# Performance work log

Measured on AMD Instinct MI355X. Metric: run time of the kernel, lower is better.

The kernel has to match this reference:

```python
import jax, jax.numpy as jnp
import numpy as np

NUM_EMBEDDINGS = 16384
EMBED_DIM = 2048
B, C, H, W = 8, EMBED_DIM, 32, 32


def setup_inputs() -> dict:
    key = jax.random.key(0)
    k1, k2 = jax.random.split(key)
    hidden_state = jax.random.normal(k1, (B, C, H, W), dtype=jnp.float32)
    embedding = jax.random.normal(k2, (NUM_EMBEDDINGS, EMBED_DIM), dtype=jnp.float32)
    return {"hidden_state": hidden_state, "embedding": embedding}


def _l2_normalize(x, axis=-1, eps=1e-12):
    # matches torch F.normalize(p=2): x / max(||x||, eps)
    n = jnp.sqrt(jnp.sum(x * x, axis=axis, keepdims=True))
    return x / jnp.maximum(n, eps)


def reference(hidden_state, embedding):
    b, c, h, w = hidden_state.shape
    # (B,C,H,W) -> (B*H*W, C)
    flat = jnp.transpose(hidden_state, (0, 2, 3, 1)).reshape(-1, c)
    z = _l2_normalize(flat)                      # [N, D]
    e = _l2_normalize(embedding)                 # [K, D]
    sim = jnp.matmul(z, e.T)                     # [N, K]
    idx = jnp.argmax(sim, axis=1)                # [N]
    quant = e[idx]                               # [N, D]
    quant = quant.reshape(b, h, w, c).transpose(0, 3, 1, 2)
    return quant, idx
```

## Files before the change

### kernel.cpp

```cpp
#include <hip/hip_runtime.h>
#include <hip/hip_bf16.h>

#define NQ   8192
#define NK   16384
#define DIM  2048
#define KTILES 128
#define QUANT_ELEMS (8*2048*32*32)

typedef __attribute__((ext_vector_type(8))) short bf16x8;
typedef __attribute__((ext_vector_type(4))) float f32x4;

__device__ __forceinline__ void async16(const void* g, void* lds) {
  __builtin_amdgcn_global_load_lds(
      (const __attribute__((address_space(1))) unsigned int*)g,
      (__attribute__((address_space(3))) unsigned int*)lds,
      16, 0, 0);
}

__device__ __forceinline__ void t2_add(float v, int i,
                                       float& v1, int& i1, float& v2, int& i2) {
  if (v > v1) { v2 = v1; i2 = i1; v1 = v; i1 = i; }
  else if (v > v2) { v2 = v; i2 = i; }
}

__global__ __launch_bounds__(256) void norm_e_kernel(
    const float* __restrict__ e, __hip_bfloat16* __restrict__ eh,
    float* __restrict__ enorm) {
  const int k = blockIdx.x;
  const int t = threadIdx.x;
  const float* row = e + (size_t)k * DIM;
  float v[8];
  double ss = 0.0;
#pragma unroll
  for (int j = 0; j < 8; j++) { v[j] = row[t + 256 * j]; ss += (double)v[j] * (double)v[j]; }
  for (int s = 32; s; s >>= 1) ss += __shfl_down(ss, s);
  __shared__ double sb[4];
  __shared__ float snorm;
  if ((t & 63) == 0) sb[t >> 6] = ss;
  __syncthreads();
  if (t == 0) {
    snorm = fmaxf((float)sqrt(sb[0] + sb[1] + sb[2] + sb[3]), 1e-12f);
    enorm[k] = snorm;
  }
  __syncthreads();
  const float nf = snorm;
#pragma unroll
  for (int j = 0; j < 8; j++)
    eh[(size_t)k * DIM + t + 256 * j] = __float2bfloat16(v[j] / nf);
}

__global__ __launch_bounds__(256) void norm_z_kernel(
    const float* __restrict__ hid, __hip_bfloat16* __restrict__ zh) {
  const int bh = blockIdx.x;
  const int b = bh >> 5, h = bh & 31;
  const int n0 = bh * 32;
  const int t = threadIdx.x;
  const int w = t & 31, cp = t >> 5;

  __shared__ double ssq[8][32];
  __shared__ float nrm[32];
  __shared__ float tile[32][65];

  double acc = 0.0;
  const float* base = hid + ((size_t)b * DIM) * 1024 + h * 32 + w;
#pragma unroll 8
  for (int k = 0; k < 256; k++) {
    float val = base[(size_t)(cp * 256 + k) * 1024];
    acc += (double)val * (double)val;
  }
  ssq[cp][w] = acc;
  __syncthreads();
  if (t < 32) {
    double s = 0.0;
#pragma unroll
    for (int j = 0; j < 8; j++) s += ssq[j][t];
    nrm[t] = fmaxf((float)sqrt(s), 1e-12f);
  }
  __syncthreads();

  for (int ct = 0; ct < 32; ct++) {
    const int c0 = ct * 64;
#pragma unroll
    for (int jt = 0; jt < 8; jt++) {
      const int cl = jt * 8 + cp;
      tile[w][cl] = base[(size_t)(c0 + cl) * 1024];
    }
    __syncthreads();
#pragma unroll
    for (int it = 0; it < 8; it++) {
      const int nl = it * 4 + (t >> 6);
      const int cl = t & 63;
      zh[(size_t)(n0 + nl) * DIM + c0 + cl] =
          __float2bfloat16(tile[nl][cl] / nrm[nl]);
    }
    __syncthreads();
  }
}

__global__ __launch_bounds__(256) void gemm_top2(
    const __hip_bfloat16* __restrict__ A, const __hip_bfloat16* __restrict__ B,
    float4* __restrict__ pertile ) {
  __shared__ __align__(16) __hip_bfloat16 As[128 * 64];
  __shared__ __align__(16) __hip_bfloat16 Bs[128 * 64];

  const int nb = blockIdx.x;
  const int kb = blockIdx.y;
  const int n0 = nb * 128;
  const int k0 = kb * 128;

  const int tid  = threadIdx.x;
  const int wid  = tid >> 6;
  const int lane = tid & 63;
  const int wm = wid >> 1, wn = wid & 1;

  const int lr = lane >> 3;
  const int sc = ((lane & 7) ^ lr) * 8;

  f32x4 acc[4][4];
#pragma unroll
  for (int i = 0; i < 4; i++)
#pragma unroll
    for (int j = 0; j < 4; j++) acc[i][j] = (f32x4){0.f, 0.f, 0.f, 0.f};

  for (int d0 = 0; d0 < DIM; d0 += 64) {
    __syncthreads();
#pragma unroll
    for (int p = 0; p < 4; p++) {
      const int row = p * 32 + wid * 8 + lr;
      const __hip_bfloat16* ga = A + (size_t)(n0 + row) * DIM + d0 + sc;
      const __hip_bfloat16* gb = B + (size_t)(k0 + row) * DIM + d0 + sc;
      async16(ga, (char*)As + p * 4096 + wid * 1024);
      async16(gb, (char*)Bs + p * 4096 + wid * 1024);
    }
    __syncthreads();
#pragma unroll
    for (int kk = 0; kk < 2; kk++) {
      bf16x8 af[4], bfr[4];
      const int cg = kk * 4 + (lane >> 4);
#pragma unroll
      for (int mi = 0; mi < 4; mi++) {
        int r = wm * 64 + mi * 16 + (lane & 15);
        af[mi] = *(const bf16x8*)(As + r * 64 + ((cg ^ (r & 7)) * 8));
      }
#pragma unroll
      for (int ni = 0; ni < 4; ni++) {
        int r = wn * 64 + ni * 16 + (lane & 15);
        bfr[ni] = *(const bf16x8*)(Bs + r * 64 + ((cg ^ (r & 7)) * 8));
      }
#pragma unroll
      for (int mi = 0; mi < 4; mi++)
#pragma unroll
        for (int ni = 0; ni < 4; ni++)
          acc[mi][ni] = __builtin_amdgcn_mfma_f32_16x16x32_bf16(
              af[mi], bfr[ni], acc[mi][ni], 0, 0, 0);
    }
  }

  __syncthreads();
  float4* buf = (float4*)As;
  const int cbase = k0 + wn * 64 + (lane & 15);
#pragma unroll
  for (int mi = 0; mi < 4; mi++) {
#pragma unroll
    for (int j = 0; j < 4; j++) {
      float v1 = -INFINITY, v2 = -INFINITY;
      int i1 = -1, i2 = -1;
#pragma unroll
      for (int ni = 0; ni < 4; ni++)
        t2_add(acc[mi][ni][j], cbase + ni * 16, v1, i1, v2, i2);
      for (int s = 1; s < 16; s <<= 1) {
        float ov1 = __shfl_xor(v1, s); int oi1 = __shfl_xor(i1, s);
        float ov2 = __shfl_xor(v2, s); int oi2 = __shfl_xor(i2, s);
        t2_add(ov1, oi1, v1, i1, v2, i2);
        t2_add(ov2, oi2, v1, i1, v2, i2);
      }
      if ((lane & 15) == 0) {
        int rl = wm * 64 + mi * 16 + ((lane >> 4) << 2) + j;
        buf[rl * 2 + wn] = make_float4(v1, v2, __int_as_float(i1), __int_as_float(i2));
      }
    }
  }
  __syncthreads();
  if (tid < 128) {
    float4 a = buf[tid * 2 + 0], b = buf[tid * 2 + 1];
    float v1 = a.x, v2 = a.y;
    int i1 = __float_as_int(a.z), i2 = __float_as_int(a.w);
    t2_add(b.x, __float_as_int(b.z), v1, i1, v2, i2);
    t2_add(b.y, __float_as_int(b.w), v1, i1, v2, i2);
    pertile[(size_t)(n0 + tid) * KTILES + kb] =
        make_float4(v1, v2, __int_as_float(i1), __int_as_float(i2));
  }
}

#define DELTA 2e-3f
__global__ __launch_bounds__(256) void rescore_kernel(
    const float4* __restrict__ pertile, const float* __restrict__ hid,
    const float* __restrict__ emb, float* __restrict__ idx_f,
    int* __restrict__ idx_i) {
  const int n = blockIdx.x;
  const int t = threadIdx.x;
  __shared__ double sredd[2][4];
  __shared__ float sm[4];
  __shared__ int sl[128];
  __shared__ int scnt;

  float4 e4 = (t < 128) ? pertile[(size_t)n * KTILES + t]
                        : make_float4(-INFINITY, -INFINITY, 0.f, 0.f);
  float m = e4.x;
  for (int s = 32; s; s >>= 1) m = fmaxf(m, __shfl_xor(m, s));
  if ((t & 63) == 0) sm[t >> 6] = m;
  __syncthreads();
  if (t == 0) {
    sm[0] = fmaxf(fmaxf(sm[0], sm[1]), fmaxf(sm[2], sm[3]));
    scnt = 0;
  }
  __syncthreads();
  const float thr = sm[0] - DELTA;
  if (t < 128) {
    if (e4.x >= thr) { int p = atomicAdd(&scnt, 1); if (p < 128) sl[p] = __float_as_int(e4.z); }
    if (e4.y >= thr) { int p = atomicAdd(&scnt, 1); if (p < 128) sl[p] = __float_as_int(e4.w); }
  }
  __syncthreads();
  const int cnt = min(scnt, 128);

  const int b = n >> 10, hw = n & 1023;
  const float* zbase = hid + (size_t)b * DIM * 1024 + hw;
  double zv[8];
#pragma unroll
  for (int j = 0; j < 8; j++) zv[j] = (double)zbase[(size_t)(t + 256 * j) * 1024];

  double bestv = -1e300;
  int besti = 0x7fffffff;
  for (int c = 0; c < cnt; c++) {
    const int k = sl[c];
    const float* erow = emb + (size_t)k * DIM;
    double dot = 0.0, ee = 0.0;
#pragma unroll
    for (int j = 0; j < 8; j++) {
      double ev = (double)erow[t + 256 * j];
      dot += zv[j] * ev;
      ee  += ev * ev;
    }
    for (int s = 32; s; s >>= 1) { dot += __shfl_down(dot, s); ee += __shfl_down(ee, s); }
    if ((t & 63) == 0) { sredd[0][t >> 6] = dot; sredd[1][t >> 6] = ee; }
    __syncthreads();
    if (t == 0) {
      double td = sredd[0][0] + sredd[0][1] + sredd[0][2] + sredd[0][3];
      double te = sredd[1][0] + sredd[1][1] + sredd[1][2] + sredd[1][3];
      double sim = td / sqrt(te);
      if (sim > bestv || (sim == bestv && k < besti)) { bestv = sim; besti = k; }
    }
    __syncthreads();
  }
  if (t == 0) { idx_f[n] = (float)besti; idx_i[n] = besti; }
}

__global__ __launch_bounds__(256) void gather_kernel(
    const float* __restrict__ emb, const float* __restrict__ enorm,
    const int* __restrict__ idx, float* __restrict__ out) {
  const int bh = blockIdx.x;
  const int b = bh >> 5, h = bh & 31;
  const int n0 = bh * 32;
  const int c0 = blockIdx.y * 64;
  const int t = threadIdx.x;

  __shared__ int rows[32];
  __shared__ float nrm[32];
  __shared__ float tile[32][65];

  if (t < 32) {
    int r = idx[n0 + t];
    rows[t] = r;
    nrm[t] = enorm[r];
  }
  __syncthreads();
#pragma unroll
  for (int it = 0; it < 8; it++) {
    const int nl = it * 4 + (t >> 6);
    const int cl = t & 63;
    tile[nl][cl] = emb[(size_t)rows[nl] * DIM + c0 + cl] / nrm[nl];
  }
  __syncthreads();
#pragma unroll
  for (int jt = 0; jt < 8; jt++) {
    const int cl = jt * 8 + (t >> 5);
    const int w = t & 31;
    out[((size_t)(b * DIM + c0 + cl) << 10) + (h << 5) + w] = tile[w][cl];
  }
}

extern "C" void kernel_launch(void* const* d_in, const int* in_sizes, int n_in,
                              void* d_out, int out_size, void* d_ws, size_t ws_size,
                              hipStream_t stream) {
  const float* hidden = (const float*)d_in[0];
  const float* emb    = (const float*)d_in[1];
  float* out = (float*)d_out;

  char* ws = (char*)d_ws;
  __hip_bfloat16* eh = (__hip_bfloat16*)ws; ws += (size_t)NK * DIM * 2;
  __hip_bfloat16* zh = (__hip_bfloat16*)ws; ws += (size_t)NQ * DIM * 2;
  float4* pertile = (float4*)ws;            ws += (size_t)NQ * KTILES * 16;
  float* enorm = (float*)ws;                ws += (size_t)NK * 4;
  int* idxi = (int*)ws;                     ws += (size_t)NQ * 4;

  norm_e_kernel<<<NK, 256, 0, stream>>>(emb, eh, enorm);
  norm_z_kernel<<<256, 256, 0, stream>>>(hidden, zh);
  gemm_top2<<<dim3(NQ / 128, KTILES), 256, 0, stream>>>(zh, eh, pertile);
  rescore_kernel<<<NQ, 256, 0, stream>>>(pertile, hidden, emb, out + QUANT_ELEMS, idxi);
  gather_kernel<<<dim3(256, DIM / 64), 256, 0, stream>>>(emb, enorm, idxi, out);
}
```

Measured before the change: 2.049 ms.

## Double-buffer LDS tiles in GEMM and swizzle block order for L2 reuse

The GEMM main loop now uses two LDS buffers, so the async global-to-LDS loads for the next 64-wide slice are issued before the MFMA work on the current slice. This removes one barrier per iteration and lets load latency overlap with compute. Block indices are also remapped so that consecutive launched blocks share N or K tiles, which should improve L2 hit rates. LDS use doubles to 64KB per block, which may reduce occupancy.

```diff
diff --git a/kernel.cpp b/kernel.cpp
--- a/kernel.cpp
+++ b/kernel.cpp
@@ -100,11 +100,13 @@
 __global__ __launch_bounds__(256) void gemm_top2(
     const __hip_bfloat16* __restrict__ A, const __hip_bfloat16* __restrict__ B,
     float4* __restrict__ pertile ) {
-  __shared__ __align__(16) __hip_bfloat16 As[128 * 64];
-  __shared__ __align__(16) __hip_bfloat16 Bs[128 * 64];
-
-  const int nb = blockIdx.x;
-  const int kb = blockIdx.y;
+  __shared__ __align__(16) __hip_bfloat16 As[2][128 * 64];
+  __shared__ __align__(16) __hip_bfloat16 Bs[2][128 * 64];
+
+  const int bid = blockIdx.x + 64 * blockIdx.y;
+  const int swz = (bid & 7) * 1024 + (bid >> 3);
+  const int nb = swz & 63;
+  const int kb = swz >> 6;
   const int n0 = nb * 128;
   const int k0 = kb * 128;
 
@@ -115,6 +117,7 @@
 
   const int lr = lane >> 3;
   const int sc = ((lane & 7) ^ lr) * 8;
+  const int srow = wid * 8 + lr;
 
   f32x4 acc[4][4];
 #pragma unroll
@@ -122,39 +125,60 @@
 #pragma unroll
     for (int j = 0; j < 4; j++) acc[i][j] = (f32x4){0.f, 0.f, 0.f, 0.f};
 
-  for (int d0 = 0; d0 < DIM; d0 += 64) {
-    __syncthreads();
-#pragma unroll
-    for (int p = 0; p < 4; p++) {
-      const int row = p * 32 + wid * 8 + lr;
-      const __hip_bfloat16* ga = A + (size_t)(n0 + row) * DIM + d0 + sc;
-      const __hip_bfloat16* gb = B + (size_t)(k0 + row) * DIM + d0 + sc;
-      async16(ga, (char*)As + p * 4096 + wid * 1024);
-      async16(gb, (char*)Bs + p * 4096 + wid * 1024);
-    }
-    __syncthreads();
-#pragma unroll
-    for (int kk = 0; kk < 2; kk++) {
-      bf16x8 af[4], bfr[4];
-      const int cg = kk * 4 + (lane >> 4);
-#pragma unroll
-      for (int mi = 0; mi < 4; mi++) {
-        int r = wm * 64 + mi * 16 + (lane & 15);
-        af[mi] = *(const bf16x8*)(As + r * 64 + ((cg ^ (r & 7)) * 8));
-      }
-#pragma unroll
-      for (int ni = 0; ni < 4; ni++) {
-        int r = wn * 64 + ni * 16 + (lane & 15);
-        bfr[ni] = *(const bf16x8*)(Bs + r * 64 + ((cg ^ (r & 7)) * 8));
-      }
-#pragma unroll
-      for (int mi = 0; mi < 4; mi++)
-#pragma unroll
-        for (int ni = 0; ni < 4; ni++)
-          acc[mi][ni] = __builtin_amdgcn_mfma_f32_16x16x32_bf16(
-              af[mi], bfr[ni], acc[mi][ni], 0, 0, 0);
-    }
-  }
+#define STAGE(bufi, d0_)                                                      \
+  do {                                                                        \
+    _Pragma("unroll")                                                         \
+    for (int p = 0; p < 4; p++) {                                             \
+      const int row = p * 32 + srow;                                          \
+      async16(A + (size_t)(n0 + row) * DIM + (d0_) + sc,                      \
+              (char*)As[bufi] + p * 4096 + wid * 1024);                       \
+      async16(B + (size_t)(k0 + row) * DIM + (d0_) + sc,                      \
+              (char*)Bs[bufi] + p * 4096 + wid * 1024);                       \
+    }                                                                         \
+  } while (0)
+
+#define COMPUTE(bufi)                                                         \
+  do {                                                                        \
+    _Pragma("unroll")                                                         \
+    for (int kk = 0; kk < 2; kk++) {                                          \
+      bf16x8 af[4], bfr[4];                                                   \
+      const int cg = kk * 4 + (lane >> 4);                                    \
+      _Pragma("unroll")                                                       \
+      for (int mi = 0; mi < 4; mi++) {                                        \
+        int r = wm * 64 + mi * 16 + (lane & 15);                              \
+        af[mi] = *(const bf16x8*)(As[bufi] + r * 64 + ((cg ^ (r & 7)) * 8));  \
+      }                                                                       \
+      _Pragma("unroll")                                                       \
+      for (int ni = 0; ni < 4; ni++) {                                        \
+        int r = wn * 64 + ni * 16 + (lane & 15);                              \
+        bfr[ni] = *(const bf16x8*)(Bs[bufi] + r * 64 + ((cg ^ (r & 7)) * 8)); \
+      }                                                                       \
+      _Pragma("unroll")                                                       \
+      for (int mi = 0; mi < 4; mi++)                                          \
+        _Pragma("unroll")                                                     \
+        for (int ni = 0; ni < 4; ni++)                                        \
+          acc[mi][ni] = __builtin_amdgcn_mfma_f32_16x16x32_bf16(              \
+              af[mi], bfr[ni], acc[mi][ni], 0, 0, 0);                         \
+    }                                                                         \
+  } while (0)
+
+  STAGE(0, 0);
+  __syncthreads();
+  for (int i = 0; i < 15; i++) {
+    const int d0 = i * 128;
+    STAGE(1, d0 + 64);
+    COMPUTE(0);
+    __syncthreads();
+    STAGE(0, d0 + 128);
+    COMPUTE(1);
+    __syncthreads();
+  }
+  STAGE(1, 1984);
+  COMPUTE(0);
+  __syncthreads();
+  COMPUTE(1);
+#undef STAGE
+#undef COMPUTE
 
   __syncthreads();
   float4* buf = (float4*)As;
```

Result: slower. 2.269 ms (+10.7%).
